# Performance work log

Hardware: AMD Instinct MI355X
Metric: run time of the kernel (lower is better)

The kernel has to match this reference:

```python
import jax, jax.numpy as jnp
import numpy as np

EMBED_DIM = 512
NUM_HEADS = 8
HEAD_DIM = EMBED_DIM // NUM_HEADS


def setup_inputs() -> dict:
    key = jax.random.key(0)
    ks = jax.random.split(key, 9)
    C = EMBED_DIM
    s = 1.0 / np.sqrt(C)
    x = jax.random.normal(ks[0], (1, 4096, C), dtype=jnp.float32)
    Wq = jax.random.uniform(ks[1], (C, C), jnp.float32, -s, s)
    bq = jax.random.uniform(ks[2], (C,), jnp.float32, -s, s)
    Wk = jax.random.uniform(ks[3], (C, C), jnp.float32, -s, s)
    bk = jax.random.uniform(ks[4], (C,), jnp.float32, -s, s)
    Wv = jax.random.uniform(ks[5], (C, C), jnp.float32, -s, s)
    bv = jax.random.uniform(ks[6], (C,), jnp.float32, -s, s)
    Wo = jax.random.uniform(ks[7], (C, C), jnp.float32, -s, s)
    bo = jax.random.uniform(ks[8], (C,), jnp.float32, -s, s)
    return {"x": x, "Wq": Wq, "bq": bq, "Wk": Wk, "bk": bk,
            "Wv": Wv, "bv": bv, "Wo": Wo, "bo": bo}


def reference(x, Wq, bq, Wk, bk, Wv, bv, Wo, bo):
    B, N, C = x.shape
    H, D = NUM_HEADS, HEAD_DIM
    # QKV projections, split into heads: [B, H, N, D]
    def proj(W, b):
        y = x @ W + b
        return y.reshape(B, N, H, D).transpose(0, 2, 1, 3)
    Q, K, V = proj(Wq, bq), proj(Wk, bk), proj(Wv, bv)
    # NOTE: original scales by 1/sqrt(embed_dim), NOT 1/sqrt(head_dim)
    scale = 1.0 / jnp.sqrt(jnp.float32(C)).astype(x.dtype)
    scores = jnp.einsum('bhnd,bhmd->bhnm', Q, K) * scale  # [B,H,N,N]
    attn = jax.nn.softmax(scores, axis=-1)
    out = jnp.einsum('bhnm,bhmd->bhnd', attn, V)  # [B,H,N,D]
    out = out.transpose(0, 2, 1, 3).reshape(B, N, C)
    return out @ Wo + bo
```

## Files before the change

kernel.cpp:

```cpp
#include <hip/hip_runtime.h>
#include <hip/hip_bf16.h>

#define SEQ 4096
#define CDIM 512
#define NHEAD 8
#define HDIM 64
#define KVB 128
#define NTI (SEQ / KVB)

typedef __attribute__((ext_vector_type(8))) short bf16x8;
typedef __attribute__((ext_vector_type(4))) float f32x4;
typedef __attribute__((ext_vector_type(16))) float f32x16;

__device__ __forceinline__ short f2b(float f) {
  union { float f; unsigned u; } v; v.f = f;
  unsigned u = v.u;
  unsigned r = u + 0x7fffu + ((u >> 16) & 1u);
  return (short)(r >> 16);
}
__device__ __forceinline__ float b2f(short s) {
  union { unsigned u; float f; } v; v.u = ((unsigned)(unsigned short)s) << 16;
  return v.f;
}
__device__ __forceinline__ unsigned pk2(float a, float b) {
  union { __hip_bfloat162 h; unsigned u; } z;
  z.h = __float22bfloat162_rn(make_float2(a, b));
  return z.u;
}

__global__ __launch_bounds__(256) void prep_kernel(
    const float* __restrict__ x,
    const float* __restrict__ Wq, const float* __restrict__ Wk,
    const float* __restrict__ Wv, const float* __restrict__ Wo,
    short* __restrict__ xb,
    short* __restrict__ Wqt, short* __restrict__ Wkt,
    short* __restrict__ Wvt, short* __restrict__ Wot) {
  __shared__ short tile[32][33];
  int b = blockIdx.x, tid = threadIdx.x;
  if (b < 2048) {
    int i = (b * 256 + tid) * 4;
    float4 v = *(const float4*)(x + i);
    short4 o;
    o.x = f2b(v.x); o.y = f2b(v.y); o.z = f2b(v.z); o.w = f2b(v.w);
    *(short4*)(xb + i) = o;
    return;
  }
  int t = b - 2048;
  int mat = t >> 8; t &= 255;
  const float* W = mat == 0 ? Wq : mat == 1 ? Wk : mat == 2 ? Wv : Wo;
  short* Wt = mat == 0 ? Wqt : mat == 1 ? Wkt : mat == 2 ? Wvt : Wot;
  int n0 = (t & 15) * 32, k0 = (t >> 4) * 32;
  int tx = tid & 31, ty = tid >> 5;
  for (int i = 0; i < 32; i += 8)
    tile[ty + i][tx] = f2b(W[(size_t)(k0 + ty + i) * CDIM + n0 + tx]);
  __syncthreads();
  for (int i = 0; i < 32; i += 8)
    Wt[(size_t)(n0 + ty + i) * CDIM + k0 + tx] = tile[tx][ty + i];
}

__global__ __launch_bounds__(256) void qkv_gemm_kernel(
    const short* __restrict__ A,
    const short* __restrict__ Wqt, const short* __restrict__ Wkt, const short* __restrict__ Wvt,
    const float* __restrict__ bq, const float* __restrict__ bk, const float* __restrict__ bv,
    short* __restrict__ Qb, short* __restrict__ Kb, short* __restrict__ Vtb) {
  __shared__ short As[64 * 64];
  __shared__ short Bs[64 * 64];
  const int z = blockIdx.z;
  const short* Bt = z == 0 ? Wqt : z == 1 ? Wkt : Wvt;
  const float* bias = z == 0 ? bq : z == 1 ? bk : bv;
  const int m0 = blockIdx.x * 64, n0 = blockIdx.y * 64;
  const int tid = threadIdx.x;
  const int w = tid >> 6, lane = tid & 63, g = lane >> 4, l16 = lane & 15;
  f32x4 acc[4] = {};
  for (int kt = 0; kt < CDIM; kt += 64) {
    __syncthreads();
    for (int it = 0; it < 2; ++it) {
      int c = tid + it * 256;
      int r = c >> 3, cc = (c & 7) * 8;
      int sw = r * 64 + (cc ^ ((r & 7) * 8));
      *(bf16x8*)(As + sw) = *(const bf16x8*)(A + (size_t)(m0 + r) * CDIM + kt + cc);
      *(bf16x8*)(Bs + sw) = *(const bf16x8*)(Bt + (size_t)(n0 + r) * CDIM + kt + cc);
    }
    __syncthreads();
    const int ar = w * 16 + l16;
    for (int ks = 0; ks < 2; ++ks) {
      int c0 = ks * 32 + 8 * g;
      bf16x8 af = *(const bf16x8*)(As + ar * 64 + (c0 ^ ((ar & 7) * 8)));
      for (int ni = 0; ni < 4; ++ni) {
        int br = ni * 16 + l16;
        bf16x8 bf = *(const bf16x8*)(Bs + br * 64 + (c0 ^ ((br & 7) * 8)));
        acc[ni] = __builtin_amdgcn_mfma_f32_16x16x32_bf16(af, bf, acc[ni], 0, 0, 0);
      }
    }
  }
  for (int ni = 0; ni < 4; ++ni) {
    int col = n0 + ni * 16 + l16;
    float bv_ = bias[col];
    for (int j = 0; j < 4; ++j) {
      int row = m0 + w * 16 + g * 4 + j;
      float v = acc[ni][j] + bv_;
      if (z == 0)      Qb[(size_t)row * CDIM + col] = f2b(v);
      else if (z == 1) Kb[(size_t)row * CDIM + col] = f2b(v);
      else             Vtb[(size_t)col * SEQ + row] = f2b(v);
    }
  }
}

__global__ __launch_bounds__(256) void out_gemm_kernel(
    const short* __restrict__ A, const short* __restrict__ Bt,
    const float* __restrict__ bias, float* __restrict__ out) {
  __shared__ short As[64 * 64];
  __shared__ short Bs[64 * 64];
  const int m0 = blockIdx.x * 64, n0 = blockIdx.y * 64;
  const int tid = threadIdx.x;
  const int w = tid >> 6, lane = tid & 63, g = lane >> 4, l16 = lane & 15;
  f32x4 acc[4] = {};
  for (int kt = 0; kt < CDIM; kt += 64) {
    __syncthreads();
    for (int it = 0; it < 2; ++it) {
      int c = tid + it * 256;
      int r = c >> 3, cc = (c & 7) * 8;
      int sw = r * 64 + (cc ^ ((r & 7) * 8));
      *(bf16x8*)(As + sw) = *(const bf16x8*)(A + (size_t)(m0 + r) * CDIM + kt + cc);
      *(bf16x8*)(Bs + sw) = *(const bf16x8*)(Bt + (size_t)(n0 + r) * CDIM + kt + cc);
    }
    __syncthreads();
    const int ar = w * 16 + l16;
    for (int ks = 0; ks < 2; ++ks) {
      int c0 = ks * 32 + 8 * g;
      bf16x8 af = *(const bf16x8*)(As + ar * 64 + (c0 ^ ((ar & 7) * 8)));
      for (int ni = 0; ni < 4; ++ni) {
        int br = ni * 16 + l16;
        bf16x8 bf = *(const bf16x8*)(Bs + br * 64 + (c0 ^ ((br & 7) * 8)));
        acc[ni] = __builtin_amdgcn_mfma_f32_16x16x32_bf16(af, bf, acc[ni], 0, 0, 0);
      }
    }
  }
  for (int ni = 0; ni < 4; ++ni) {
    int col = n0 + ni * 16 + l16;
    float bv_ = bias[col];
    for (int j = 0; j < 4; ++j) {
      int row = m0 + w * 16 + g * 4 + j;
      out[(size_t)row * CDIM + col] = acc[ni][j] + bv_;
    }
  }
}

__global__ __launch_bounds__(512, 4) void attn_kernel(
    const short* __restrict__ Qb,
    const short* __restrict__ Kb,
    const short* __restrict__ Vtb,
    short* __restrict__ Ob) {
  __shared__ __align__(16) short Ks[2][KVB * 64];
  __shared__ __align__(16) short Vs[2][64 * KVB];
  __shared__ float lz[4][2][32];
  const int bid = blockIdx.x;
  const int h = bid & 7;
  const int q0 = (bid >> 3) * 64;
  const int tid = threadIdx.x;
  const int wid = tid >> 6, lane = tid & 63;
  const int l31 = lane & 31, hi = lane >> 5;
  const int rh = wid >> 2, kq = wid & 3;
  const float scale2 = 0.06375872274f;

  bf16x8 qf[4];
  {
    int qrow = q0 + rh * 32 + l31;
#pragma unroll
    for (int kst = 0; kst < 4; ++kst) {
      bf16x8 q = *(const bf16x8*)(Qb + (size_t)qrow * CDIM + h * 64 + kst * 16 + hi * 8);
#pragma unroll
      for (int i = 0; i < 8; ++i) q[i] = f2b(b2f(q[i]) * scale2);
      qf[kst] = q;
    }
  }

  const int krow_ = tid >> 3;
  const int kcol_ = 8 * ((tid & 7) ^ ((tid >> 3) & 7));
  const int vrow_ = tid >> 4;
  const int vcol_ = 8 * ((tid & 15) ^ ((tid >> 4) & 7));
  auto stage = [&](int buf, int kv0) {
#pragma unroll
    for (int it = 0; it < 2; ++it) {
      __builtin_amdgcn_global_load_lds(
          (const __attribute__((address_space(1))) void*)(
              Kb + (size_t)(kv0 + krow_ + it * 64) * CDIM + h * 64 + kcol_),
          (__attribute__((address_space(3))) void*)(&Ks[buf][tid * 8 + it * 4096]), 16, 0, 0);
      __builtin_amdgcn_global_load_lds(
          (const __attribute__((address_space(1))) void*)(
              Vtb + (size_t)(h * 64 + vrow_ + it * 32) * SEQ + kv0 + vcol_),
          (__attribute__((address_space(3))) void*)(&Vs[buf][tid * 8 + it * 4096]), 16, 0, 0);
    }
  };

  f32x16 osum[2] = {};
  float lsum = 0.f;

  stage(0, 0);
  __syncthreads();

  int cur = 0;
  for (int t = 0; t < NTI; ++t) {
    if (t + 1 < NTI) stage(cur ^ 1, (t + 1) * KVB);

    const short* ks_lds = &Ks[cur][0];
    const short* vs_lds = &Vs[cur][0];

    f32x16 s = {};
    __builtin_amdgcn_s_setprio(1);
#pragma unroll
    for (int kst = 0; kst < 4; ++kst) {
      int row = kq * 32 + l31;
      bf16x8 kf = *(const bf16x8*)(ks_lds + row * 64 + ((kst * 16 + hi * 8) ^ ((row & 7) * 8)));
      s = __builtin_amdgcn_mfma_f32_32x32x16_bf16(kf, qf[kst], s, 0, 0, 0);
    }
    __builtin_amdgcn_s_setprio(0);

    float p[16];
#pragma unroll
    for (int r = 0; r < 16; ++r) {
      p[r] = __builtin_amdgcn_exp2f(s[r]);
      lsum += p[r];
    }
    unsigned w[8];
#pragma unroll
    for (int m = 0; m < 8; ++m) w[m] = pk2(p[2 * m], p[2 * m + 1]);

#pragma unroll
    for (int ks2 = 0; ks2 < 2; ++ks2) {
      unsigned t0 = hi ? w[4 * ks2 + 0] : w[4 * ks2 + 2];
      unsigned t1 = hi ? w[4 * ks2 + 1] : w[4 * ks2 + 3];
      unsigned r0 = __shfl_xor(t0, 32);
      unsigned r1 = __shfl_xor(t1, 32);
      union { unsigned u[4]; bf16x8 v; } pf;
      pf.u[0] = hi ? r0 : w[4 * ks2 + 0];
      pf.u[1] = hi ? r1 : w[4 * ks2 + 1];
      pf.u[2] = hi ? w[4 * ks2 + 2] : r0;
      pf.u[3] = hi ? w[4 * ks2 + 3] : r1;
      __builtin_amdgcn_s_setprio(1);
#pragma unroll
      for (int dm = 0; dm < 2; ++dm) {
        int vrow = dm * 32 + l31;
        bf16x8 vf = *(const bf16x8*)(
            vs_lds + vrow * KVB + ((kq * 32 + ks2 * 16 + hi * 8) ^ ((vrow & 7) * 8)));
        osum[dm] = __builtin_amdgcn_mfma_f32_32x32x16_bf16(vf, pf.v, osum[dm], 0, 0, 0);
      }
      __builtin_amdgcn_s_setprio(0);
    }

    __syncthreads();
    cur ^= 1;
  }

  lsum += __shfl_xor(lsum, 32);

  __syncthreads();
  float* bufA = (float*)&Ks[0][0];
  float* bufB = (float*)&Vs[0][0];
  if (hi == 0) lz[kq][rh][l31] = lsum;

#define OD(dm, r) ((dm) * 32 + ((r) & 3) + 8 * ((r) >> 2) + 4 * hi)
#define OADDR(dm, r) (rh * 2112 + OD(dm, r) * 33 + l31)

  if (kq == 1 || kq == 3) {
    float* z = (kq == 1) ? bufA : bufB;
#pragma unroll
    for (int dm = 0; dm < 2; ++dm)
#pragma unroll
      for (int r = 0; r < 16; ++r) z[OADDR(dm, r)] = osum[dm][r];
  }
  __syncthreads();
  if (kq == 0) {
#pragma unroll
    for (int dm = 0; dm < 2; ++dm)
#pragma unroll
      for (int r = 0; r < 16; ++r) osum[dm][r] += bufA[OADDR(dm, r)];
  } else if (kq == 2) {
#pragma unroll
    for (int dm = 0; dm < 2; ++dm)
#pragma unroll
      for (int r = 0; r < 16; ++r) {
        osum[dm][r] += bufB[OADDR(dm, r)];
        bufB[OADDR(dm, r)] = osum[dm][r];
      }
  }
  __syncthreads();
  if (kq == 0) {
#pragma unroll
    for (int dm = 0; dm < 2; ++dm)
#pragma unroll
      for (int r = 0; r < 16; ++r) bufA[OADDR(dm, r)] = osum[dm][r] + bufB[OADDR(dm, r)];
  }
  __syncthreads();

  {
    int q_ = tid >> 3;
    int dc = (tid & 7) * 8;
    int qr = q_ >> 5, ql = q_ & 31;
    float l4 = lz[0][qr][ql] + lz[1][qr][ql] + lz[2][qr][ql] + lz[3][qr][ql];
    float rinv = 1.f / l4;
    short ov[8];
#pragma unroll
    for (int i = 0; i < 8; ++i)
      ov[i] = f2b(bufA[qr * 2112 + (dc + i) * 33 + ql] * rinv);
    *(bf16x8*)(Ob + (size_t)(q0 + q_) * CDIM + h * 64 + dc) = *(bf16x8*)ov;
  }
#undef OD
#undef OADDR
}

extern "C" void kernel_launch(void* const* d_in, const int* in_sizes, int n_in,
                              void* d_out, int out_size, void* d_ws, size_t ws_size,
                              hipStream_t stream) {
  const float* x  = (const float*)d_in[0];
  const float* Wq = (const float*)d_in[1];
  const float* bq = (const float*)d_in[2];
  const float* Wk = (const float*)d_in[3];
  const float* bk = (const float*)d_in[4];
  const float* Wv = (const float*)d_in[5];
  const float* bv = (const float*)d_in[6];
  const float* Wo = (const float*)d_in[7];
  const float* bo = (const float*)d_in[8];
  float* out = (float*)d_out;

  short* ws = (short*)d_ws;
  size_t off = 0;
  short* xb  = ws + off; off += (size_t)SEQ * CDIM;
  short* Wqt = ws + off; off += (size_t)CDIM * CDIM;
  short* Wkt = ws + off; off += (size_t)CDIM * CDIM;
  short* Wvt = ws + off; off += (size_t)CDIM * CDIM;
  short* Wot = ws + off; off += (size_t)CDIM * CDIM;
  short* Qb  = ws + off; off += (size_t)SEQ * CDIM;
  short* Kb  = ws + off; off += (size_t)SEQ * CDIM;
  short* Vtb = ws + off; off += (size_t)CDIM * SEQ;
  short* Ab  = ws + off; off += (size_t)SEQ * CDIM;

  prep_kernel<<<2048 + 4 * 256, 256, 0, stream>>>(x, Wq, Wk, Wv, Wo, xb, Wqt, Wkt, Wvt, Wot);
  qkv_gemm_kernel<<<dim3(SEQ / 64, CDIM / 64, 3), 256, 0, stream>>>(
      xb, Wqt, Wkt, Wvt, bq, bk, bv, Qb, Kb, Vtb);
  attn_kernel<<<(SEQ / 64) * NHEAD, 512, 0, stream>>>(Qb, Kb, Vtb, Ab);
  out_gemm_kernel<<<dim3(SEQ / 64, CDIM / 64), 256, 0, stream>>>(Ab, Wot, bo, out);
}
```

Before: 87.91 us.

## Split attention across KV into four partitions with a separate combine kernel

Restructures attention as a split-KV (flash-decoding style) scheme. Each block now handles 128 queries over one quarter of the sequence with 64-row KV tiles and 2 KV warps per query group. It writes unnormalized bf16 partial outputs and fp32 row sums, and a new combine kernel adds the four partials and normalizes. The goal is more blocks, higher occupancy (launch bounds 8) and less LDS. The cost is an extra kernel launch, extra global traffic for the partials, and bf16 rounding of the partials before combining. It also swaps the cross-half lane shuffle for permlane32_swap when that builtin exists.

```diff
diff --git a/kernel.cpp b/kernel.cpp
--- a/kernel.cpp
+++ b/kernel.cpp
@@ -5,8 +5,9 @@
 #define CDIM 512
 #define NHEAD 8
 #define HDIM 64
-#define KVB 128
-#define NTI (SEQ / KVB)
+#define KVB 64
+#define NSPLIT 4
+#define TILES_PER_SPLIT (SEQ / KVB / NSPLIT)
 
 typedef __attribute__((ext_vector_type(8))) short bf16x8;
 typedef __attribute__((ext_vector_type(4))) float f32x4;
@@ -146,22 +147,30 @@
   }
 }
 
-__global__ __launch_bounds__(512, 4) void attn_kernel(
+__global__ __launch_bounds__(512, 8) void attn_kernel(
     const short* __restrict__ Qb,
     const short* __restrict__ Kb,
     const short* __restrict__ Vtb,
-    short* __restrict__ Ob) {
-  __shared__ __align__(16) short Ks[2][KVB * 64];
-  __shared__ __align__(16) short Vs[2][64 * KVB];
-  __shared__ float lz[4][2][32];
+    short* __restrict__ Op0, short* __restrict__ Op1,
+    short* __restrict__ Op2, short* __restrict__ Op3,
+    float* __restrict__ lpart) {
+  __shared__ __align__(16) char arena[33792];
+  __shared__ float lzp[4][32];
+  short* KsB = (short*)arena;
+  short* VsB = (short*)(arena + 16384);
   const int bid = blockIdx.x;
   const int h = bid & 7;
-  const int q0 = (bid >> 3) * 64;
+  const int rest = bid >> 3;
+  const int split = rest & 3;
+  const int q0 = (rest >> 2) * 128;
+  const int kvbase = split * (TILES_PER_SPLIT * KVB);
   const int tid = threadIdx.x;
   const int wid = tid >> 6, lane = tid & 63;
   const int l31 = lane & 31, hi = lane >> 5;
-  const int rh = wid >> 2, kq = wid & 3;
+  const int rh = wid >> 1, kq = wid & 1;
   const float scale2 = 0.06375872274f;
+
+  short* Opart = split == 0 ? Op0 : split == 1 ? Op1 : split == 2 ? Op2 : Op3;
 
   bf16x8 qf[4];
   {
@@ -175,36 +184,31 @@
     }
   }
 
-  const int krow_ = tid >> 3;
-  const int kcol_ = 8 * ((tid & 7) ^ ((tid >> 3) & 7));
-  const int vrow_ = tid >> 4;
-  const int vcol_ = 8 * ((tid & 15) ^ ((tid >> 4) & 7));
+  const int srow = tid >> 3;
+  const int scol8 = 8 * ((tid & 7) ^ (srow & 7));
   auto stage = [&](int buf, int kv0) {
-#pragma unroll
-    for (int it = 0; it < 2; ++it) {
-      __builtin_amdgcn_global_load_lds(
-          (const __attribute__((address_space(1))) void*)(
-              Kb + (size_t)(kv0 + krow_ + it * 64) * CDIM + h * 64 + kcol_),
-          (__attribute__((address_space(3))) void*)(&Ks[buf][tid * 8 + it * 4096]), 16, 0, 0);
-      __builtin_amdgcn_global_load_lds(
-          (const __attribute__((address_space(1))) void*)(
-              Vtb + (size_t)(h * 64 + vrow_ + it * 32) * SEQ + kv0 + vcol_),
-          (__attribute__((address_space(3))) void*)(&Vs[buf][tid * 8 + it * 4096]), 16, 0, 0);
-    }
+    __builtin_amdgcn_global_load_lds(
+        (const __attribute__((address_space(1))) void*)(
+            Kb + (size_t)(kv0 + srow) * CDIM + h * 64 + scol8),
+        (__attribute__((address_space(3))) void*)(&KsB[buf * 4096 + tid * 8]), 16, 0, 0);
+    __builtin_amdgcn_global_load_lds(
+        (const __attribute__((address_space(1))) void*)(
+            Vtb + (size_t)(h * 64 + srow) * SEQ + kv0 + scol8),
+        (__attribute__((address_space(3))) void*)(&VsB[buf * 4096 + tid * 8]), 16, 0, 0);
   };
 
   f32x16 osum[2] = {};
   float lsum = 0.f;
 
-  stage(0, 0);
+  stage(0, kvbase);
   __syncthreads();
 
   int cur = 0;
-  for (int t = 0; t < NTI; ++t) {
-    if (t + 1 < NTI) stage(cur ^ 1, (t + 1) * KVB);
-
-    const short* ks_lds = &Ks[cur][0];
-    const short* vs_lds = &Vs[cur][0];
+  for (int t = 0; t < TILES_PER_SPLIT; ++t) {
+    if (t + 1 < TILES_PER_SPLIT) stage(cur ^ 1, kvbase + (t + 1) * KVB);
+
+    const short* ks_lds = KsB + cur * 4096;
+    const short* vs_lds = VsB + cur * 4096;
 
     f32x16 s = {};
     __builtin_amdgcn_s_setprio(1);
@@ -216,33 +220,44 @@
     }
     __builtin_amdgcn_s_setprio(0);
 
-    float p[16];
-#pragma unroll
-    for (int r = 0; r < 16; ++r) {
-      p[r] = __builtin_amdgcn_exp2f(s[r]);
-      lsum += p[r];
-    }
     unsigned w[8];
-#pragma unroll
-    for (int m = 0; m < 8; ++m) w[m] = pk2(p[2 * m], p[2 * m + 1]);
+    float ls0 = 0.f, ls1 = 0.f;
+#pragma unroll
+    for (int m = 0; m < 8; ++m) {
+      float p0 = __builtin_amdgcn_exp2f(s[2 * m]);
+      float p1 = __builtin_amdgcn_exp2f(s[2 * m + 1]);
+      ls0 += p0; ls1 += p1;
+      w[m] = pk2(p0, p1);
+    }
+    lsum += ls0 + ls1;
 
 #pragma unroll
     for (int ks2 = 0; ks2 < 2; ++ks2) {
-      unsigned t0 = hi ? w[4 * ks2 + 0] : w[4 * ks2 + 2];
-      unsigned t1 = hi ? w[4 * ks2 + 1] : w[4 * ks2 + 3];
-      unsigned r0 = __shfl_xor(t0, 32);
-      unsigned r1 = __shfl_xor(t1, 32);
       union { unsigned u[4]; bf16x8 v; } pf;
-      pf.u[0] = hi ? r0 : w[4 * ks2 + 0];
-      pf.u[1] = hi ? r1 : w[4 * ks2 + 1];
-      pf.u[2] = hi ? w[4 * ks2 + 2] : r0;
-      pf.u[3] = hi ? w[4 * ks2 + 3] : r1;
+#if __has_builtin(__builtin_amdgcn_permlane32_swap)
+      {
+        auto sw0 = __builtin_amdgcn_permlane32_swap(w[4 * ks2 + 0], w[4 * ks2 + 2], false, false);
+        auto sw1 = __builtin_amdgcn_permlane32_swap(w[4 * ks2 + 1], w[4 * ks2 + 3], false, false);
+        pf.u[0] = sw0[0]; pf.u[1] = sw1[0]; pf.u[2] = sw0[1]; pf.u[3] = sw1[1];
+      }
+#else
+      {
+        unsigned t0 = hi ? w[4 * ks2 + 0] : w[4 * ks2 + 2];
+        unsigned t1 = hi ? w[4 * ks2 + 1] : w[4 * ks2 + 3];
+        unsigned r0 = __shfl_xor(t0, 32);
+        unsigned r1 = __shfl_xor(t1, 32);
+        pf.u[0] = hi ? r0 : w[4 * ks2 + 0];
+        pf.u[1] = hi ? r1 : w[4 * ks2 + 1];
+        pf.u[2] = hi ? w[4 * ks2 + 2] : r0;
+        pf.u[3] = hi ? w[4 * ks2 + 3] : r1;
+      }
+#endif
       __builtin_amdgcn_s_setprio(1);
 #pragma unroll
       for (int dm = 0; dm < 2; ++dm) {
         int vrow = dm * 32 + l31;
         bf16x8 vf = *(const bf16x8*)(
-            vs_lds + vrow * KVB + ((kq * 32 + ks2 * 16 + hi * 8) ^ ((vrow & 7) * 8)));
+            vs_lds + vrow * 64 + ((kq * 32 + ks2 * 16 + hi * 8) ^ ((vrow & 7) * 8)));
         osum[dm] = __builtin_amdgcn_mfma_f32_32x32x16_bf16(vf, pf.v, osum[dm], 0, 0, 0);
       }
       __builtin_amdgcn_s_setprio(0);
@@ -255,58 +270,67 @@
   lsum += __shfl_xor(lsum, 32);
 
   __syncthreads();
-  float* bufA = (float*)&Ks[0][0];
-  float* bufB = (float*)&Vs[0][0];
-  if (hi == 0) lz[kq][rh][l31] = lsum;
-
+  float* bufA = (float*)arena;
 #define OD(dm, r) ((dm) * 32 + ((r) & 3) + 8 * ((r) >> 2) + 4 * hi)
 #define OADDR(dm, r) (rh * 2112 + OD(dm, r) * 33 + l31)
-
-  if (kq == 1 || kq == 3) {
-    float* z = (kq == 1) ? bufA : bufB;
+  if (kq == 1) {
+    if (hi == 0) lzp[rh][l31] = lsum;
 #pragma unroll
     for (int dm = 0; dm < 2; ++dm)
 #pragma unroll
-      for (int r = 0; r < 16; ++r) z[OADDR(dm, r)] = osum[dm][r];
+      for (int r = 0; r < 16; ++r) bufA[OADDR(dm, r)] = osum[dm][r];
   }
   __syncthreads();
   if (kq == 0) {
 #pragma unroll
     for (int dm = 0; dm < 2; ++dm)
 #pragma unroll
-      for (int r = 0; r < 16; ++r) osum[dm][r] += bufA[OADDR(dm, r)];
-  } else if (kq == 2) {
-#pragma unroll
-    for (int dm = 0; dm < 2; ++dm)
-#pragma unroll
       for (int r = 0; r < 16; ++r) {
-        osum[dm][r] += bufB[OADDR(dm, r)];
-        bufB[OADDR(dm, r)] = osum[dm][r];
-      }
-  }
-  __syncthreads();
-  if (kq == 0) {
-#pragma unroll
-    for (int dm = 0; dm < 2; ++dm)
-#pragma unroll
-      for (int r = 0; r < 16; ++r) bufA[OADDR(dm, r)] = osum[dm][r] + bufB[OADDR(dm, r)];
-  }
-  __syncthreads();
-
-  {
-    int q_ = tid >> 3;
-    int dc = (tid & 7) * 8;
-    int qr = q_ >> 5, ql = q_ & 31;
-    float l4 = lz[0][qr][ql] + lz[1][qr][ql] + lz[2][qr][ql] + lz[3][qr][ql];
-    float rinv = 1.f / l4;
-    short ov[8];
-#pragma unroll
-    for (int i = 0; i < 8; ++i)
-      ov[i] = f2b(bufA[qr * 2112 + (dc + i) * 33 + ql] * rinv);
-    *(bf16x8*)(Ob + (size_t)(q0 + q_) * CDIM + h * 64 + dc) = *(bf16x8*)ov;
-  }
+        float v = osum[dm][r] + bufA[OADDR(dm, r)];
+        bufA[OADDR(dm, r)] = v;
+      }
+    float lt = lsum + lzp[rh][l31];
+    if (hi == 0)
+      lpart[(size_t)(split * NHEAD + h) * SEQ + q0 + rh * 32 + l31] = lt;
+  }
+  __syncthreads();
 #undef OD
 #undef OADDR
+
+  {
+    int q_ = tid >> 2;
+    int dc = (tid & 3) * 16;
+    int qr = q_ >> 5, ql = q_ & 31;
+    short ov[16];
+#pragma unroll
+    for (int i = 0; i < 16; ++i)
+      ov[i] = f2b(bufA[qr * 2112 + (dc + i) * 33 + ql]);
+    *(bf16x8*)(Opart + (size_t)(q0 + q_) * CDIM + h * 64 + dc) = *(bf16x8*)(ov);
+    *(bf16x8*)(Opart + (size_t)(q0 + q_) * CDIM + h * 64 + dc + 8) = *(bf16x8*)(ov + 8);
+  }
+}
+
+__global__ __launch_bounds__(256) void combine_kernel(
+    const short* __restrict__ p0, const short* __restrict__ p1,
+    const short* __restrict__ p2, const short* __restrict__ p3,
+    const float* __restrict__ lpart, short* __restrict__ Ab) {
+  int t = blockIdx.x * 256 + threadIdx.x;
+  size_t base = (size_t)t * 8;
+  int q = (int)(base >> 9), c = (int)(base & 511), h = c >> 6;
+  float l = lpart[(size_t)(0 * NHEAD + h) * SEQ + q] +
+            lpart[(size_t)(1 * NHEAD + h) * SEQ + q] +
+            lpart[(size_t)(2 * NHEAD + h) * SEQ + q] +
+            lpart[(size_t)(3 * NHEAD + h) * SEQ + q];
+  float rinv = 1.f / l;
+  bf16x8 a0 = *(const bf16x8*)(p0 + base);
+  bf16x8 a1 = *(const bf16x8*)(p1 + base);
+  bf16x8 a2 = *(const bf16x8*)(p2 + base);
+  bf16x8 a3 = *(const bf16x8*)(p3 + base);
+  short ov[8];
+#pragma unroll
+  for (int i = 0; i < 8; ++i)
+    ov[i] = f2b((b2f(a0[i]) + b2f(a1[i]) + b2f(a2[i]) + b2f(a3[i])) * rinv);
+  *(bf16x8*)(Ab + base) = *(bf16x8*)(ov);
 }
 
 extern "C" void kernel_launch(void* const* d_in, const int* in_sizes, int n_in,
@@ -334,10 +358,17 @@
   short* Kb  = ws + off; off += (size_t)SEQ * CDIM;
   short* Vtb = ws + off; off += (size_t)CDIM * SEQ;
   short* Ab  = ws + off; off += (size_t)SEQ * CDIM;
+  short* Op1 = ws + off; off += (size_t)SEQ * CDIM;
+  short* Op2 = ws + off; off += (size_t)SEQ * CDIM;
+  short* Op3 = ws + off; off += (size_t)SEQ * CDIM;
+  float* lpart = (float*)(ws + off); off += (size_t)NSPLIT * NHEAD * SEQ * 2;
+  short* Op0 = xb;
 
   prep_kernel<<<2048 + 4 * 256, 256, 0, stream>>>(x, Wq, Wk, Wv, Wo, xb, Wqt, Wkt, Wvt, Wot);
   qkv_gemm_kernel<<<dim3(SEQ / 64, CDIM / 64, 3), 256, 0, stream>>>(
       xb, Wqt, Wkt, Wvt, bq, bk, bv, Qb, Kb, Vtb);
-  attn_kernel<<<(SEQ / 64) * NHEAD, 512, 0, stream>>>(Qb, Kb, Vtb, Ab);
+  attn_kernel<<<(SEQ / 128) * NHEAD * NSPLIT, 512, 0, stream>>>(
+      Qb, Kb, Vtb, Op0, Op1, Op2, Op3, lpart);
+  combine_kernel<<<SEQ * CDIM / 8 / 256, 256, 0, stream>>>(Op0, Op1, Op2, Op3, lpart, Ab);
   out_gemm_kernel<<<dim3(SEQ / 64, CDIM / 64), 256, 0, stream>>>(Ab, Wot, bo, out);
 }
```

New measurement: 176.2 us. +100.4%, slower.
